# Kernel optimization log

Measured on AMD Instinct MI355X. Metric: run time of the kernel, lower is better.

## Reference

```python
import jax, jax.numpy as jnp
import numpy as np


def setup_inputs() -> dict:
    key = jax.random.key(0)
    k_u, k_wl, k_b, k_c = jax.random.split(key, 4)
    B_, T, D, N = 4, 4096, 1024, 256
    u = jax.random.normal(k_u, (B_, T, D), dtype=jnp.float32)
    # torch init: W_lambda.weight zeros, bias 2.0; B, C xavier_uniform gain=0.5.
    # Use small random weights for W_lambda too so the path is exercised.
    Wl = jax.random.normal(k_wl, (N, D), dtype=jnp.float32) * 0.02
    bl = jnp.full((N,), 2.0, dtype=jnp.float32)
    xav_b = 0.5 * np.sqrt(6.0 / (D + N))
    Wb = jax.random.uniform(k_b, (N, D), dtype=jnp.float32, minval=-xav_b, maxval=xav_b)
    xav_c = 0.5 * np.sqrt(6.0 / (N + D))
    Wc = jax.random.uniform(k_c, (D, N), dtype=jnp.float32, minval=-xav_c, maxval=xav_c)
    Dp = jnp.zeros((D,), dtype=jnp.float32)
    return {"u": u, "Wl": Wl, "bl": bl, "Wb": Wb, "Wc": Wc, "Dp": Dp}


def reference(u, Wl, bl, Wb, Wc, Dp):
    # u: (B, T, D). Precompute per-step gates and inputs with batched GEMMs,
    # then run the diagonal linear recurrence with lax.scan over time.
    lam = jax.nn.sigmoid(jnp.einsum('btd,nd->btn', u, Wl) + bl)  # (B, T, N)
    Bu = jnp.einsum('btd,nd->btn', u, Wb)                         # (B, T, N)

    def step(h, inp):
        lam_t, bu_t = inp            # each (B, N)
        h = lam_t * h + bu_t
        return h, h

    h0 = jnp.zeros((u.shape[0], Wl.shape[0]), dtype=u.dtype)
    # scan over time: move T to leading axis
    _, H = jax.lax.scan(step, h0, (jnp.swapaxes(lam, 0, 1), jnp.swapaxes(Bu, 0, 1)))
    H = jnp.swapaxes(H, 0, 1)        # (B, T, N)
    y = jnp.einsum('btn,dn->btd', H, Wc) + u * Dp
    return y
```

## Files before the change

kernel.cpp:

```cpp
#include <hip/hip_runtime.h>


typedef __bf16 bf16_t;
typedef __attribute__((ext_vector_type(8))) __bf16 bf16x8;
typedef __attribute__((ext_vector_type(4))) __bf16 bf16x4;
typedef __attribute__((ext_vector_type(4))) float f32x4;

#define B_  4
#define T_  4096
#define D_  1024
#define N_  256
#define BT  (B_ * T_)
#define NCHUNK 64
#define CHLEN  (T_ / NCHUNK)

#define GLOAD_LDS16(g, l) __builtin_amdgcn_global_load_lds(              \
    (__attribute__((address_space(1))) void*)(g),                        \
    (__attribute__((address_space(3))) void*)(l), 16, 0, 0)

__global__ void cvt_f32_bf16(const float* __restrict__ in,
                             bf16_t* __restrict__ out, int n4) {
  int i = blockIdx.x * 256 + threadIdx.x;
  if (i >= n4) return;
  float4 v = ((const float4*)in)[i];
  bf16x4 o = {(__bf16)v.x, (__bf16)v.y, (__bf16)v.z, (__bf16)v.w};
  ((bf16x4*)out)[i] = o;
}

__global__ void cvt_wcomb(const float* __restrict__ Wl,
                          const float* __restrict__ Wb,
                          bf16_t* __restrict__ out) {
  int i = blockIdx.x * 256 + threadIdx.x;
  int e = i * 4;
  int j = e >> 10;
  int d = e & 1023;
  const float* src = (j < 256) ? (Wl + (size_t)j * D_ + d)
                               : (Wb + (size_t)(j - 256) * D_ + d);
  float4 v = *(const float4*)src;
  bf16x4 o = {(__bf16)v.x, (__bf16)v.y, (__bf16)v.z, (__bf16)v.w};
  ((bf16x4*)out)[i] = o;
}

__device__ __forceinline__ void mfma_tile8(const bf16_t* bufA, const bf16_t* bufB,
                                           int wr, int wc, int r16, int kq,
                                           f32x4 (&acc)[4][2]) {
  const int sw = (r16 & 7) << 3;
#pragma unroll
  for (int kk = 0; kk < 2; ++kk) {
    bf16x8 af[4], bfr[2];
#pragma unroll
    for (int m = 0; m < 4; ++m) {
      int idx = (wr * 64 + m * 16 + r16) * 64 + kk * 32 + kq * 8;
      af[m] = *(const bf16x8*)&bufA[idx ^ sw];
    }
#pragma unroll
    for (int n = 0; n < 2; ++n) {
      int idx = (wc * 32 + n * 16 + r16) * 64 + kk * 32 + kq * 8;
      bfr[n] = *(const bf16x8*)&bufB[idx ^ sw];
    }
#pragma unroll
    for (int m = 0; m < 4; ++m)
#pragma unroll
      for (int n = 0; n < 2; ++n)
        acc[m][n] = __builtin_amdgcn_mfma_f32_16x16x32_bf16(af[m], bfr[n], acc[m][n], 0, 0, 0);
  }
}

__global__ __launch_bounds__(512, 4)
void gemm1_kernel(const float* __restrict__ A, const bf16_t* __restrict__ Bm,
                  float* __restrict__ C, const float* __restrict__ bl) {
  __shared__ bf16_t lA[2][128 * 64];
  __shared__ bf16_t lB[2][128 * 64];
  const int wid  = threadIdx.x >> 6;
  const int lane = threadIdx.x & 63;
  const int work = (blockIdx.x & 7) * 64 + (blockIdx.x >> 3);
  const int brow = work >> 2;
  const int bcol = work & 3;
  const int r16 = lane & 15;
  const int kq  = lane >> 4;
  const int wr = wid >> 2, wc = wid & 3;

  f32x4 acc[4][2] = {};

  const int ar = lane >> 4;
  const int ac = (lane & 15) * 4;
  const float* gA = A + (size_t)(brow * 128 + wid * 16 + ar) * D_ + ac;
  const int aw_base = (wid * 16 + ar) * 64 + ac;

  const bf16_t* gB = Bm + (size_t)(bcol * 128 + wid * 16 + (lane >> 3)) * D_
                        + (size_t)(((lane & 7) ^ (lane >> 3)) * 8);

  {
    float4 va[4];
#pragma unroll
    for (int i = 0; i < 4; ++i)
      va[i] = *(const float4*)(gA + (size_t)(i * 4) * D_);
#pragma unroll
    for (int i = 0; i < 2; ++i)
      GLOAD_LDS16(gB + (size_t)(i * 8) * D_, &lB[0][(wid * 16 + i * 8) * 64]);
#pragma unroll
    for (int i = 0; i < 4; ++i) {
      bf16x4 o = {(__bf16)va[i].x, (__bf16)va[i].y,
                  (__bf16)va[i].z, (__bf16)va[i].w};
      int idx = (aw_base + i * 4 * 64) ^ (((ar + 4 * (i & 1)) & 7) << 3);
      *(bf16x4*)&lA[0][idx] = o;
    }
    __syncthreads();
  }

  int cur = 0;
#pragma unroll 1
  for (int k0 = 0; k0 < D_ - 64; k0 += 64) {
    float4 va[4];
#pragma unroll
    for (int i = 0; i < 4; ++i)
      va[i] = *(const float4*)(gA + (size_t)(i * 4) * D_ + k0 + 64);
#pragma unroll
    for (int i = 0; i < 2; ++i)
      GLOAD_LDS16(gB + (size_t)(i * 8) * D_ + k0 + 64,
                  &lB[cur ^ 1][(wid * 16 + i * 8) * 64]);
    mfma_tile8(lA[cur], lB[cur], wr, wc, r16, kq, acc);
#pragma unroll
    for (int i = 0; i < 4; ++i) {
      bf16x4 o = {(__bf16)va[i].x, (__bf16)va[i].y,
                  (__bf16)va[i].z, (__bf16)va[i].w};
      int idx = (aw_base + i * 4 * 64) ^ (((ar + 4 * (i & 1)) & 7) << 3);
      *(bf16x4*)&lA[cur ^ 1][idx] = o;
    }
    __syncthreads();
    cur ^= 1;
  }
  mfma_tile8(lA[cur], lB[cur], wr, wc, r16, kq, acc);

#pragma unroll
  for (int m = 0; m < 4; ++m) {
#pragma unroll
    for (int n = 0; n < 2; ++n) {
      int row0 = brow * 128 + wr * 64 + m * 16 + kq * 4;
      int col  = bcol * 128 + wc * 32 + n * 16 + r16;
#pragma unroll
      for (int j = 0; j < 4; ++j) {
        float v = acc[m][n][j];
        int row = row0 + j;
        if (col < 256) v = 1.0f / (1.0f + __expf(-(v + bl[col])));
        C[(size_t)row * 512 + col] = v;
      }
    }
  }
}

__global__ __launch_bounds__(512, 4)
void gemm2_kernel(const bf16_t* __restrict__ A, const bf16_t* __restrict__ Bm,
                  float* __restrict__ C,
                  const float* __restrict__ u, const float* __restrict__ Dp) {
  __shared__ bf16_t lA[2][128 * 64];
  __shared__ bf16_t lB[2][128 * 64];
  const int wid  = threadIdx.x >> 6;
  const int lane = threadIdx.x & 63;
  const int brow = blockIdx.x;
  const int bcol = blockIdx.y;
  const int r16 = lane & 15;
  const int kq  = lane >> 4;
  const int wr = wid >> 2, wc = wid & 3;

  f32x4 acc[4][2] = {};

  const size_t scol = ((lane & 7) ^ (lane >> 3)) * 8;
  const bf16_t* gA = A + (size_t)(brow * 128 + wid * 16 + (lane >> 3)) * N_ + scol;
  const bf16_t* gB = Bm + (size_t)(bcol * 128 + wid * 16 + (lane >> 3)) * N_ + scol;

  {
#pragma unroll
    for (int i = 0; i < 2; ++i) {
      GLOAD_LDS16(gA + (size_t)(i * 8) * N_, &lA[0][(wid * 16 + i * 8) * 64]);
      GLOAD_LDS16(gB + (size_t)(i * 8) * N_, &lB[0][(wid * 16 + i * 8) * 64]);
    }
    __syncthreads();
  }
  int cur = 0;
#pragma unroll 1
  for (int k0 = 0; k0 < N_ - 64; k0 += 64) {
#pragma unroll
    for (int i = 0; i < 2; ++i) {
      GLOAD_LDS16(gA + (size_t)(i * 8) * N_ + k0 + 64,
                  &lA[cur ^ 1][(wid * 16 + i * 8) * 64]);
      GLOAD_LDS16(gB + (size_t)(i * 8) * N_ + k0 + 64,
                  &lB[cur ^ 1][(wid * 16 + i * 8) * 64]);
    }
    mfma_tile8(lA[cur], lB[cur], wr, wc, r16, kq, acc);
    __syncthreads();
    cur ^= 1;
  }
  mfma_tile8(lA[cur], lB[cur], wr, wc, r16, kq, acc);

#pragma unroll
  for (int m = 0; m < 4; ++m) {
#pragma unroll
    for (int n = 0; n < 2; ++n) {
      int row0 = brow * 128 + wr * 64 + m * 16 + kq * 4;
      int col  = bcol * 128 + wc * 32 + n * 16 + r16;
#pragma unroll
      for (int j = 0; j < 4; ++j) {
        int row = row0 + j;
        float v = acc[m][n][j] + Dp[col] * u[(size_t)row * D_ + col];
        C[(size_t)row * D_ + col] = v;
      }
    }
  }
}

__global__ void scan_phase1(const float* __restrict__ Z,
                            float* __restrict__ wsA, float* __restrict__ wsB) {
  int tid = blockIdx.x * 256 + threadIdx.x;
  int n = tid & 255;
  int chunk = (tid >> 8) & (NCHUNK - 1);
  int b = tid >> 14;
  const float* zl = Z + ((size_t)(b * T_ + chunk * CHLEN)) * 512 + n;
  float A = 1.f, h = 0.f;
#pragma unroll 8
  for (int t = 0; t < CHLEN; ++t) {
    float lam = zl[0];
    float bu  = zl[256];
    A *= lam;
    h = fmaf(lam, h, bu);
    zl += 512;
  }
  wsA[tid] = A;
  wsB[tid] = h;
}

__global__ void scan_phase2(const float* __restrict__ wsA,
                            const float* __restrict__ wsB,
                            float* __restrict__ carry) {
  int tid = blockIdx.x * 256 + threadIdx.x;
  int n = tid & 255;
  int b = tid >> 8;
  float h = 0.f;
#pragma unroll
  for (int c = 0; c < NCHUNK; ++c) {
    int idx = (b * NCHUNK + c) * 256 + n;
    carry[idx] = h;
    h = fmaf(wsA[idx], h, wsB[idx]);
  }
}

__global__ void scan_phase3(const float* __restrict__ Z,
                            const float* __restrict__ carry,
                            bf16_t* __restrict__ H) {
  int tid = blockIdx.x * 256 + threadIdx.x;
  int n = tid & 255;
  int chunk = (tid >> 8) & (NCHUNK - 1);
  int b = tid >> 14;
  const float* zl = Z + ((size_t)(b * T_ + chunk * CHLEN)) * 512 + n;
  bf16_t* ho = H + ((size_t)(b * T_ + chunk * CHLEN)) * 256 + n;
  float h = carry[tid];
#pragma unroll 8
  for (int t = 0; t < CHLEN; ++t) {
    float lam = zl[0];
    float bu  = zl[256];
    h = fmaf(lam, h, bu);
    *ho = (__bf16)h;
    zl += 512;
    ho += 256;
  }
}

extern "C" void kernel_launch(void* const* d_in, const int* in_sizes, int n_in,
                              void* d_out, int out_size, void* d_ws, size_t ws_size,
                              hipStream_t stream) {
  const float* u  = (const float*)d_in[0];
  const float* Wl = (const float*)d_in[1];
  const float* bl = (const float*)d_in[2];
  const float* Wb = (const float*)d_in[3];
  const float* Wc = (const float*)d_in[4];
  const float* Dp = (const float*)d_in[5];
  float* y = (float*)d_out;

  char* ws = (char*)d_ws;
  float*  Z     = (float*)(ws + 0);
  bf16_t* H     = (bf16_t*)(ws + 33554432);
  bf16_t* Wcomb = (bf16_t*)(ws + 41943040);
  bf16_t* Wc_bf = (bf16_t*)(ws + 42991616);
  float*  wsA   = (float*)(ws + 43515904);
  float*  wsB   = (float*)(ws + 43778048);
  float*  carry = (float*)(ws + 44040192);

  cvt_wcomb<<<(512 * D_ / 4) / 256, 256, 0, stream>>>(Wl, Wb, Wcomb);
  cvt_f32_bf16<<<(D_ * N_ / 4) / 256, 256, 0, stream>>>(Wc, Wc_bf, D_ * N_ / 4);

  gemm1_kernel<<<512, 512, 0, stream>>>(u, Wcomb, Z, bl);

  scan_phase1<<<(B_ * NCHUNK * N_) / 256, 256, 0, stream>>>(Z, wsA, wsB);
  scan_phase2<<<(B_ * N_) / 256, 256, 0, stream>>>(wsA, wsB, carry);
  scan_phase3<<<(B_ * NCHUNK * N_) / 256, 256, 0, stream>>>(Z, carry, H);

  dim3 g2(BT / 128, D_ / 128);
  gemm2_kernel<<<g2, 512, 0, stream>>>(H, Wc_bf, y, u, Dp);
}
```

Before: 200.6 us.

## Store gates and inputs as bf16, vectorize scan, double chunks, merge weight casts

```diff
diff --git a/kernel.cpp b/kernel.cpp
--- a/kernel.cpp
+++ b/kernel.cpp
@@ -11,34 +11,34 @@
 #define D_  1024
 #define N_  256
 #define BT  (B_ * T_)
-#define NCHUNK 64
+#define NCHUNK 128
 #define CHLEN  (T_ / NCHUNK)
 
 #define GLOAD_LDS16(g, l) __builtin_amdgcn_global_load_lds(              \
     (__attribute__((address_space(1))) void*)(g),                        \
     (__attribute__((address_space(3))) void*)(l), 16, 0, 0)
 
-__global__ void cvt_f32_bf16(const float* __restrict__ in,
-                             bf16_t* __restrict__ out, int n4) {
+__global__ void cvt_weights(const float* __restrict__ Wl,
+                            const float* __restrict__ Wb,
+                            const float* __restrict__ Wc,
+                            bf16_t* __restrict__ Wcomb,
+                            bf16_t* __restrict__ Wc_bf) {
   int i = blockIdx.x * 256 + threadIdx.x;
-  if (i >= n4) return;
-  float4 v = ((const float4*)in)[i];
-  bf16x4 o = {(__bf16)v.x, (__bf16)v.y, (__bf16)v.z, (__bf16)v.w};
-  ((bf16x4*)out)[i] = o;
-}
-
-__global__ void cvt_wcomb(const float* __restrict__ Wl,
-                          const float* __restrict__ Wb,
-                          bf16_t* __restrict__ out) {
-  int i = blockIdx.x * 256 + threadIdx.x;
-  int e = i * 4;
-  int j = e >> 10;
-  int d = e & 1023;
-  const float* src = (j < 256) ? (Wl + (size_t)j * D_ + d)
-                               : (Wb + (size_t)(j - 256) * D_ + d);
-  float4 v = *(const float4*)src;
-  bf16x4 o = {(__bf16)v.x, (__bf16)v.y, (__bf16)v.z, (__bf16)v.w};
-  ((bf16x4*)out)[i] = o;
+  if (i < 131072) {
+    int e = i * 4;
+    int j = e >> 10;
+    int d = e & 1023;
+    const float* src = (j < 256) ? (Wl + (size_t)j * D_ + d)
+                                 : (Wb + (size_t)(j - 256) * D_ + d);
+    float4 v = *(const float4*)src;
+    bf16x4 o = {(__bf16)v.x, (__bf16)v.y, (__bf16)v.z, (__bf16)v.w};
+    ((bf16x4*)Wcomb)[i] = o;
+  } else {
+    int k = i - 131072;
+    float4 v = ((const float4*)Wc)[k];
+    bf16x4 o = {(__bf16)v.x, (__bf16)v.y, (__bf16)v.z, (__bf16)v.w};
+    ((bf16x4*)Wc_bf)[k] = o;
+  }
 }
 
 __device__ __forceinline__ void mfma_tile8(const bf16_t* bufA, const bf16_t* bufB,
@@ -68,7 +68,8 @@
 
 __global__ __launch_bounds__(512, 4)
 void gemm1_kernel(const float* __restrict__ A, const bf16_t* __restrict__ Bm,
-                  float* __restrict__ C, const float* __restrict__ bl) {
+                  bf16_t* __restrict__ Lam, bf16_t* __restrict__ Bu,
+                  const float* __restrict__ bl) {
   __shared__ bf16_t lA[2][128 * 64];
   __shared__ bf16_t lB[2][128 * 64];
   const int wid  = threadIdx.x >> 6;
@@ -142,8 +143,12 @@
       for (int j = 0; j < 4; ++j) {
         float v = acc[m][n][j];
         int row = row0 + j;
-        if (col < 256) v = 1.0f / (1.0f + __expf(-(v + bl[col])));
-        C[(size_t)row * 512 + col] = v;
+        if (bcol < 2) {
+          v = 1.0f / (1.0f + __expf(-(v + bl[col])));
+          Lam[(size_t)row * N_ + col] = (__bf16)v;
+        } else {
+          Bu[(size_t)row * N_ + (col - 256)] = (__bf16)v;
+        }
       }
     }
   }
@@ -209,24 +214,31 @@
   }
 }
 
-__global__ void scan_phase1(const float* __restrict__ Z,
-                            float* __restrict__ wsA, float* __restrict__ wsB) {
-  int tid = blockIdx.x * 256 + threadIdx.x;
-  int n = tid & 255;
-  int chunk = (tid >> 8) & (NCHUNK - 1);
-  int b = tid >> 14;
-  const float* zl = Z + ((size_t)(b * T_ + chunk * CHLEN)) * 512 + n;
-  float A = 1.f, h = 0.f;
+__global__ __launch_bounds__(64)
+void scan_phase1(const bf16_t* __restrict__ Lam, const bf16_t* __restrict__ Bu,
+                 float* __restrict__ wsA, float* __restrict__ wsB) {
+  int tid = blockIdx.x * 64 + threadIdx.x;
+  int ng = tid & 31;
+  int chunk = (tid >> 5) & (NCHUNK - 1);
+  int b = tid >> 12;
+  size_t base = ((size_t)(b * T_ + chunk * CHLEN)) * N_ + ng * 8;
+  float A[8], h[8];
+#pragma unroll
+  for (int i = 0; i < 8; ++i) { A[i] = 1.f; h[i] = 0.f; }
 #pragma unroll 8
   for (int t = 0; t < CHLEN; ++t) {
-    float lam = zl[0];
-    float bu  = zl[256];
-    A *= lam;
-    h = fmaf(lam, h, bu);
-    zl += 512;
-  }
-  wsA[tid] = A;
-  wsB[tid] = h;
+    bf16x8 lv = *(const bf16x8*)&Lam[base + (size_t)t * N_];
+    bf16x8 bv = *(const bf16x8*)&Bu[base + (size_t)t * N_];
+#pragma unroll
+    for (int i = 0; i < 8; ++i) {
+      float l = (float)lv[i];
+      A[i] *= l;
+      h[i] = fmaf(l, h[i], (float)bv[i]);
+    }
+  }
+  size_t o = ((size_t)(b * NCHUNK + chunk)) * N_ + ng * 8;
+#pragma unroll
+  for (int i = 0; i < 8; ++i) { wsA[o + i] = A[i]; wsB[o + i] = h[i]; }
 }
 
 __global__ void scan_phase2(const float* __restrict__ wsA,
@@ -236,32 +248,37 @@
   int n = tid & 255;
   int b = tid >> 8;
   float h = 0.f;
-#pragma unroll
+#pragma unroll 8
   for (int c = 0; c < NCHUNK; ++c) {
-    int idx = (b * NCHUNK + c) * 256 + n;
+    size_t idx = ((size_t)(b * NCHUNK + c)) * N_ + n;
     carry[idx] = h;
     h = fmaf(wsA[idx], h, wsB[idx]);
   }
 }
 
-__global__ void scan_phase3(const float* __restrict__ Z,
-                            const float* __restrict__ carry,
-                            bf16_t* __restrict__ H) {
-  int tid = blockIdx.x * 256 + threadIdx.x;
-  int n = tid & 255;
-  int chunk = (tid >> 8) & (NCHUNK - 1);
-  int b = tid >> 14;
-  const float* zl = Z + ((size_t)(b * T_ + chunk * CHLEN)) * 512 + n;
-  bf16_t* ho = H + ((size_t)(b * T_ + chunk * CHLEN)) * 256 + n;
-  float h = carry[tid];
+__global__ __launch_bounds__(64)
+void scan_phase3(const bf16_t* __restrict__ Lam, const bf16_t* __restrict__ Bu,
+                 const float* __restrict__ carry, bf16_t* __restrict__ H) {
+  int tid = blockIdx.x * 64 + threadIdx.x;
+  int ng = tid & 31;
+  int chunk = (tid >> 5) & (NCHUNK - 1);
+  int b = tid >> 12;
+  size_t base = ((size_t)(b * T_ + chunk * CHLEN)) * N_ + ng * 8;
+  size_t o = ((size_t)(b * NCHUNK + chunk)) * N_ + ng * 8;
+  float h[8];
+#pragma unroll
+  for (int i = 0; i < 8; ++i) h[i] = carry[o + i];
 #pragma unroll 8
   for (int t = 0; t < CHLEN; ++t) {
-    float lam = zl[0];
-    float bu  = zl[256];
-    h = fmaf(lam, h, bu);
-    *ho = (__bf16)h;
-    zl += 512;
-    ho += 256;
+    bf16x8 lv = *(const bf16x8*)&Lam[base + (size_t)t * N_];
+    bf16x8 bv = *(const bf16x8*)&Bu[base + (size_t)t * N_];
+    bf16x8 hv;
+#pragma unroll
+    for (int i = 0; i < 8; ++i) {
+      h[i] = fmaf((float)lv[i], h[i], (float)bv[i]);
+      hv[i] = (__bf16)h[i];
+    }
+    *(bf16x8*)&H[base + (size_t)t * N_] = hv;
   }
 }
 
@@ -277,22 +294,22 @@
   float* y = (float*)d_out;
 
   char* ws = (char*)d_ws;
-  float*  Z     = (float*)(ws + 0);
-  bf16_t* H     = (bf16_t*)(ws + 33554432);
-  bf16_t* Wcomb = (bf16_t*)(ws + 41943040);
-  bf16_t* Wc_bf = (bf16_t*)(ws + 42991616);
-  float*  wsA   = (float*)(ws + 43515904);
-  float*  wsB   = (float*)(ws + 43778048);
-  float*  carry = (float*)(ws + 44040192);
-
-  cvt_wcomb<<<(512 * D_ / 4) / 256, 256, 0, stream>>>(Wl, Wb, Wcomb);
-  cvt_f32_bf16<<<(D_ * N_ / 4) / 256, 256, 0, stream>>>(Wc, Wc_bf, D_ * N_ / 4);
-
-  gemm1_kernel<<<512, 512, 0, stream>>>(u, Wcomb, Z, bl);
-
-  scan_phase1<<<(B_ * NCHUNK * N_) / 256, 256, 0, stream>>>(Z, wsA, wsB);
-  scan_phase2<<<(B_ * N_) / 256, 256, 0, stream>>>(wsA, wsB, carry);
-  scan_phase3<<<(B_ * NCHUNK * N_) / 256, 256, 0, stream>>>(Z, carry, H);
+  bf16_t* Lam   = (bf16_t*)(ws + 0);
+  bf16_t* Bu    = (bf16_t*)(ws + 8388608);
+  bf16_t* H     = (bf16_t*)(ws + 16777216);
+  bf16_t* Wcomb = (bf16_t*)(ws + 25165824);
+  bf16_t* Wc_bf = (bf16_t*)(ws + 26214400);
+  float*  wsA   = (float*)(ws + 26738688);
+  float*  wsB   = (float*)(ws + 27262976);
+  float*  carry = (float*)(ws + 27787264);
+
+  cvt_weights<<<768, 256, 0, stream>>>(Wl, Wb, Wc, Wcomb, Wc_bf);
+
+  gemm1_kernel<<<512, 512, 0, stream>>>(u, Wcomb, Lam, Bu, bl);
+
+  scan_phase1<<<256, 64, 0, stream>>>(Lam, Bu, wsA, wsB);
+  scan_phase2<<<4, 256, 0, stream>>>(wsA, wsB, carry);
+  scan_phase3<<<256, 64, 0, stream>>>(Lam, Bu, carry, H);
 
   dim3 g2(BT / 128, D_ / 128);
   gemm2_kernel<<<g2, 512, 0, stream>>>(H, Wc_bf, y, u, Dp);
```

Result: slower. 206.2 us (+2.8%).
